# Kernel optimization log

Measured on AMD Instinct MI355X. Metric: run time of the kernel, lower is better.

Reference implementation:

```python
import jax, jax.numpy as jnp
import numpy as np

HEADS = 12
DIM = 768
DH = DIM // HEADS


def setup_inputs() -> dict:
    key = jax.random.key(0)
    k1, k2 = jax.random.split(key)
    z = jax.random.normal(k1, (4, 2048, DIM), dtype=jnp.float32)
    # nn.Linear(dim, 3*dim, bias=False): weight shape [3*dim, dim], y = z @ W.T
    W_qkv = jax.random.normal(k2, (3 * DIM, DIM), dtype=jnp.float32) * (1.0 / np.sqrt(DIM))
    return {"z": z, "W_qkv": W_qkv}


def reference(z, W_qkv):
    b, n, d = z.shape
    qkv = jnp.einsum('bnd,ed->bne', z, W_qkv)  # [b, n, 3*dim]
    # last dim layout is (headNum, m, Dh) per the einops pattern '(headNum m Dh)'
    qkv = qkv.reshape(b, n, HEADS, 3, DH)
    q = jnp.transpose(qkv[:, :, :, 0, :], (0, 2, 1, 3))  # [b, h, n, Dh]
    k = jnp.transpose(qkv[:, :, :, 1, :], (0, 2, 1, 3))
    v = jnp.transpose(qkv[:, :, :, 2, :], (0, 2, 1, 3))
    scores = jnp.einsum('bhqd,bhkd->bhqk', q, k) / np.sqrt(DH).astype(np.float32)
    A = jax.nn.softmax(scores, axis=-1)  # full [b, h, n, n] matrix, as in source
    out = jnp.einsum('bhqk,bhkd->bhqd', A, v)  # [b, h, n, Dh]
    return jnp.transpose(out, (0, 2, 1, 3)).reshape(b, n, d)
```

## Files before the change

kernel.cpp:

```cpp
#include <hip/hip_runtime.h>
#include <hip/hip_bf16.h>
#include <stdint.h>


typedef __attribute__((ext_vector_type(8))) short bf8_t;
typedef __attribute__((ext_vector_type(4))) float f4_t;

__device__ __forceinline__ unsigned short f2bf(float f) {
  union { float f; unsigned u; } x; x.f = f;
  return (unsigned short)((x.u + 0x7fffu + ((x.u >> 16) & 1u)) >> 16);
}
__device__ __forceinline__ unsigned cvt_pk_bf16(float lo, float hi) {
  unsigned r;
  asm("v_cvt_pk_bf16_f32 %0, %1, %2" : "=v"(r) : "v"(lo), "v"(hi));
  return r;
}
__device__ __forceinline__ void gload_lds16(const void* g, void* l) {
  __builtin_amdgcn_global_load_lds(
      (const __attribute__((address_space(1))) void*)g,
      (__attribute__((address_space(3))) void*)l, 16, 0, 0);
}

__global__ __launch_bounds__(256) void cvt_kernel(
    const float* __restrict__ Z, const float* __restrict__ W,
    unsigned short* __restrict__ Zb)
{
  const int idx = blockIdx.x * 256 + threadIdx.x;
  const float* src;
  unsigned short* dst;
  int c;
  if (idx < 786432) { src = Z; dst = Zb; c = idx; }
  else              { src = W; dst = Zb + 6291456; c = idx - 786432; }
  const float4 a0 = *(const float4*)(src + (size_t)c * 8);
  const float4 a1 = *(const float4*)(src + (size_t)c * 8 + 4);
  uint4 pk = { cvt_pk_bf16(a0.x, a0.y), cvt_pk_bf16(a0.z, a0.w),
               cvt_pk_bf16(a1.x, a1.y), cvt_pk_bf16(a1.z, a1.w) };
  *(uint4*)(dst + (size_t)c * 8) = pk;
}

__global__ __launch_bounds__(256, 3) void qkv_gemm_kernel(
    const unsigned short* __restrict__ Zb, const unsigned short* __restrict__ Wb,
    unsigned short* __restrict__ qb, unsigned short* __restrict__ kb,
    unsigned short* __restrict__ vt)
{
  __shared__ __align__(16) unsigned short As[128 * 64];
  __shared__ __align__(16) unsigned short Bs[128 * 64];

  const int tid = threadIdx.x;
  const int w    = tid >> 6;
  const int lane = tid & 63;
  const int g    = lane >> 4;
  const int l15  = lane & 15;
  const int bid0 = blockIdx.y * 18 + blockIdx.x;
  const int bid  = (bid0 & 7) * 144 + (bid0 >> 3);
  const int m0 = (bid / 18) * 128;
  const int n0 = (bid % 18) * 128;
  const int wr = w >> 1, wc = w & 1;

  const int arow = w * 32 + (lane >> 3);
  const int achk = ((lane & 7) ^ (lane >> 3)) * 8;
  const unsigned short* za = Zb + (size_t)(m0 + arow) * 768 + achk;
  const unsigned short* wa = Wb + (size_t)(n0 + arow) * 768 + achk;
  unsigned short* const lza = As + w * 32 * 64;
  unsigned short* const lwa = Bs + w * 32 * 64;

  const f4_t zf = {0.f, 0.f, 0.f, 0.f};
  f4_t acc[4][4];
#pragma unroll
  for (int m = 0; m < 4; ++m)
#pragma unroll
    for (int n = 0; n < 4; ++n) acc[m][n] = zf;

  for (int ks = 0; ks < 12; ++ks) {
    __syncthreads();
#pragma unroll
    for (int r = 0; r < 4; ++r) {
      gload_lds16(za + r * 8 * 768, lza + r * 512);
      gload_lds16(wa + r * 8 * 768, lwa + r * 512);
    }
    za += 64; wa += 64;
    __syncthreads();

#pragma unroll
    for (int s = 0; s < 2; ++s) {
      bf8_t af[4], bfr[4];
#pragma unroll
      for (int m = 0; m < 4; ++m) {
        const int row = wr * 64 + m * 16 + l15;
        af[m] = *(const bf8_t*)(As + row * 64 + (((s * 4 + g) ^ (row & 7)) * 8));
      }
#pragma unroll
      for (int n = 0; n < 4; ++n) {
        const int row = wc * 64 + n * 16 + l15;
        bfr[n] = *(const bf8_t*)(Bs + row * 64 + (((s * 4 + g) ^ (row & 7)) * 8));
      }
      __builtin_amdgcn_s_setprio(1);
#pragma unroll
      for (int m = 0; m < 4; ++m)
#pragma unroll
        for (int n = 0; n < 4; ++n)
          acc[m][n] = __builtin_amdgcn_mfma_f32_16x16x32_bf16(af[m], bfr[n], acc[m][n], 0, 0, 0);
      __builtin_amdgcn_s_setprio(0);
    }
  }

  const float QSCALE = 0.18033688011112042f;
#pragma unroll
  for (int m = 0; m < 4; ++m) {
    const int gi  = m0 + wr * 64 + m * 16 + g * 4;
    const int b   = gi >> 11;
    const int tok = gi & 2047;
#pragma unroll
    for (int n = 0; n < 4; ++n) {
      const int e0  = n0 + wc * 64 + n * 16;
      const int h   = e0 / 192;
      const int rem = e0 - h * 192;
      const int mm  = rem >> 6;
      const int dh  = (rem & 63) + l15;
      if (mm == 2) {
        uint2 pk = { cvt_pk_bf16(acc[m][n][0], acc[m][n][1]),
                     cvt_pk_bf16(acc[m][n][2], acc[m][n][3]) };
        const int pos = ((tok >> 5) & 1) * 32 + ((tok >> 2) & 3) * 8
                      + ((tok >> 4) & 1) * 4;
        const size_t vaddr = ((size_t)(b * 12 + h) * 32 + (tok >> 6)) * 4096
                           + dh * 64 + pos;
        *(uint2*)(vt + vaddr) = pk;
      } else {
        unsigned short* buf = mm ? kb : qb;
        const float sc = mm ? 1.0f : QSCALE;
        const size_t base = ((size_t)((b * 12 + h) * 2048 + tok)) * 64 + dh;
#pragma unroll
        for (int j = 0; j < 4; ++j)
          buf[base + (size_t)j * 64] = f2bf(acc[m][n][j] * sc);
      }
    }
  }
}

__global__ __launch_bounds__(256, 3) void attn_kernel(
    const unsigned short* __restrict__ qb, const unsigned short* __restrict__ kb,
    const unsigned short* __restrict__ vt, float* __restrict__ out)
{
  __shared__ __align__(16) unsigned short Ks[2][64 * 64];
  __shared__ __align__(16) unsigned short Vs[2][64 * 64];

  const int bid = blockIdx.x;
  const int nb  = (bid & 7) * 96 + (bid >> 3);
  const int bh  = nb >> 4;
  const int qt  = nb & 15;
  const int tid = threadIdx.x;
  const int w    = tid >> 6;
  const int lane = tid & 63;
  const int g    = lane >> 4;
  const int l15  = lane & 15;

  const unsigned short* Qh  = qb + (size_t)bh * 2048 * 64;
  const unsigned short* Kh  = kb + (size_t)bh * 2048 * 64;
  const unsigned short* VTh = vt + (size_t)bh * 32 * 4096;

  const int qbase = qt * 128 + w * 32;

  bf8_t qfr[2][2];
#pragma unroll
  for (int qq = 0; qq < 2; ++qq)
#pragma unroll
    for (int s = 0; s < 2; ++s)
      qfr[qq][s] = *(const bf8_t*)(Qh + (size_t)(qbase + qq * 16 + l15) * 64 + s * 32 + g * 8);

  const int xk   = l15 & 7;
  const int offA = l15 * 64 + ((g) ^ xk) * 8;
  const int offB = l15 * 64 + ((4 + g) ^ xk) * 8;

  const size_t dmaoff = (size_t)(w * 16 + (lane >> 3)) * 64
                      + ((lane & 7) ^ (lane >> 3)) * 8;
  const unsigned short* ksrc = Kh + dmaoff;
  const unsigned short* vsrc = VTh + dmaoff;
  const int ldsoff = w * 16 * 64;

  gload_lds16(ksrc,                 &Ks[0][ldsoff]);
  gload_lds16(ksrc + 8 * 64,        &Ks[0][ldsoff + 8 * 64]);
  gload_lds16(vsrc,                 &Vs[0][ldsoff]);
  gload_lds16(vsrc + 8 * 64,        &Vs[0][ldsoff + 8 * 64]);
  gload_lds16(ksrc + 4096,          &Ks[1][ldsoff]);
  gload_lds16(ksrc + 4096 + 8 * 64, &Ks[1][ldsoff + 8 * 64]);
  gload_lds16(vsrc + 4096,          &Vs[1][ldsoff]);
  gload_lds16(vsrc + 4096 + 8 * 64, &Vs[1][ldsoff + 8 * 64]);
  __syncthreads();

  const unsigned short* kdma = ksrc + 2 * 4096;
  const unsigned short* vdma = vsrc + 2 * 4096;

  const f4_t m16 = {-16.f, -16.f, -16.f, -16.f};
  const f4_t zf  = {0.f, 0.f, 0.f, 0.f};
  f4_t accO[2][4];
  unsigned pw[2][8];
  float lsumP[2] = {0.f, 0.f};
#pragma unroll
  for (int qq = 0; qq < 2; ++qq)
#pragma unroll
    for (int nf = 0; nf < 4; ++nf) accO[qq][nf] = zf;

  {
    const unsigned short* pK = &Ks[0][0];
    bf8_t ka0[4][2];
#pragma unroll
    for (int kf = 0; kf < 4; ++kf) {
      ka0[kf][0] = *(const bf8_t*)(pK + offA + kf * 1024);
      ka0[kf][1] = *(const bf8_t*)(pK + offB + kf * 1024);
    }
#pragma unroll
    for (int qq = 0; qq < 2; ++qq) {
      f4_t accS[4];
      __builtin_amdgcn_s_setprio(1);
#pragma unroll
      for (int kf = 0; kf < 4; ++kf) {
        f4_t a = __builtin_amdgcn_mfma_f32_16x16x32_bf16(ka0[kf][0], qfr[qq][0], m16, 0, 0, 0);
        accS[kf] = __builtin_amdgcn_mfma_f32_16x16x32_bf16(ka0[kf][1], qfr[qq][1], a, 0, 0, 0);
      }
      __builtin_amdgcn_s_setprio(0);
      float ps = 0.f;
#pragma unroll
      for (int kf = 0; kf < 4; ++kf) {
        const float p0 = __builtin_amdgcn_exp2f(accS[kf][0]);
        const float p1 = __builtin_amdgcn_exp2f(accS[kf][1]);
        const float p2 = __builtin_amdgcn_exp2f(accS[kf][2]);
        const float p3 = __builtin_amdgcn_exp2f(accS[kf][3]);
        ps += (p0 + p1) + (p2 + p3);
        pw[qq][kf * 2]     = cvt_pk_bf16(p0, p1);
        pw[qq][kf * 2 + 1] = cvt_pk_bf16(p2, p3);
      }
      lsumP[qq] += ps;
    }
  }

  for (int t = 0; t < 32; ++t) {
    const int cur = t & 1;
    const unsigned short* pV = &Vs[cur][0];

    bf8_t vfr[2][4];
#pragma unroll
    for (int nf = 0; nf < 4; ++nf) {
      vfr[0][nf] = *(const bf8_t*)(pV + offA + nf * 1024);
      vfr[1][nf] = *(const bf8_t*)(pV + offB + nf * 1024);
    }

    __syncthreads();

    if (t < 30) {
      gload_lds16(kdma,          &Ks[cur][ldsoff]);
      gload_lds16(kdma + 8 * 64, &Ks[cur][ldsoff + 8 * 64]);
      gload_lds16(vdma,          &Vs[cur][ldsoff]);
      gload_lds16(vdma + 8 * 64, &Vs[cur][ldsoff + 8 * 64]);
      kdma += 4096; vdma += 4096;
    }

    bf8_t ka[4][2];
    if (t < 31) {
      const unsigned short* pK = &Ks[cur ^ 1][0];
#pragma unroll
      for (int kf = 0; kf < 4; ++kf) {
        ka[kf][0] = *(const bf8_t*)(pK + offA + kf * 1024);
        ka[kf][1] = *(const bf8_t*)(pK + offB + kf * 1024);
      }
    }

    __builtin_amdgcn_s_setprio(1);
#pragma unroll
    for (int qq = 0; qq < 2; ++qq) {
      union { bf8_t v[2]; unsigned u[8]; } pa;
#pragma unroll
      for (int i = 0; i < 8; ++i) pa.u[i] = pw[qq][i];
#pragma unroll
      for (int kk = 0; kk < 2; ++kk)
#pragma unroll
        for (int nf = 0; nf < 4; ++nf)
          accO[qq][nf] = __builtin_amdgcn_mfma_f32_16x16x32_bf16(pa.v[kk], vfr[kk][nf], accO[qq][nf], 0, 0, 0);
    }
    __builtin_amdgcn_s_setprio(0);

    if (t < 31) {
#pragma unroll
      for (int qq = 0; qq < 2; ++qq) {
        f4_t accS[4];
        __builtin_amdgcn_s_setprio(1);
#pragma unroll
        for (int kf = 0; kf < 4; ++kf) {
          f4_t a = __builtin_amdgcn_mfma_f32_16x16x32_bf16(ka[kf][0], qfr[qq][0], m16, 0, 0, 0);
          accS[kf] = __builtin_amdgcn_mfma_f32_16x16x32_bf16(ka[kf][1], qfr[qq][1], a, 0, 0, 0);
        }
        __builtin_amdgcn_s_setprio(0);
        float ps = 0.f;
#pragma unroll
        for (int kf = 0; kf < 4; ++kf) {
          const float p0 = __builtin_amdgcn_exp2f(accS[kf][0]);
          const float p1 = __builtin_amdgcn_exp2f(accS[kf][1]);
          const float p2 = __builtin_amdgcn_exp2f(accS[kf][2]);
          const float p3 = __builtin_amdgcn_exp2f(accS[kf][3]);
          ps += (p0 + p1) + (p2 + p3);
          pw[qq][kf * 2]     = cvt_pk_bf16(p0, p1);
          pw[qq][kf * 2 + 1] = cvt_pk_bf16(p2, p3);
        }
        lsumP[qq] += ps;
      }
    }
  }

  const int b = bh / 12, h = bh - (bh / 12) * 12;
#pragma unroll
  for (int qq = 0; qq < 2; ++qq) {
    float ls = lsumP[qq];
    ls += __shfl_xor(ls, 16);
    ls += __shfl_xor(ls, 32);
    const float rl = 1.0f / ls;
    f4_t lv;
#pragma unroll
    for (int j = 0; j < 4; ++j) lv[j] = __shfl(rl, g * 4 + j);
#pragma unroll
    for (int nf = 0; nf < 4; ++nf) {
#pragma unroll
      for (int j = 0; j < 4; ++j) {
        const int qrow = qbase + qq * 16 + g * 4 + j;
        out[((size_t)(b * 2048 + qrow)) * 768 + h * 64 + nf * 16 + l15] = accO[qq][nf][j] * lv[j];
      }
    }
  }
}

extern "C" void kernel_launch(void* const* d_in, const int* in_sizes, int n_in,
                              void* d_out, int out_size, void* d_ws, size_t ws_size,
                              hipStream_t stream) {
  (void)in_sizes; (void)n_in; (void)out_size; (void)ws_size;
  const float* Z = (const float*)d_in[0];
  const float* W = (const float*)d_in[1];
  float* out = (float*)d_out;

  unsigned short* qb = (unsigned short*)d_ws;
  unsigned short* kb = qb + (size_t)48 * 2048 * 64;
  unsigned short* vt = kb + (size_t)48 * 2048 * 64;

  unsigned short* Zb = (unsigned short*)d_out;
  unsigned short* Wb = Zb + (size_t)8192 * 768;

  cvt_kernel<<<dim3(3936), 256, 0, stream>>>(Z, W, Zb);
  qkv_gemm_kernel<<<dim3(18, 64), 256, 0, stream>>>(Zb, Wb, qb, kb, vt);
  attn_kernel<<<dim3(768), 256, 0, stream>>>(qb, kb, vt, out);
}
```

Measured before the change: 104.4 us.

## Double-buffer LDS tiles in QKV GEMM to overlap global loads with MFMA

The QKV projection GEMM now uses two LDS buffers per operand. Two K-stages are preloaded, and each iteration reads all fragments into registers, then issues the async global-to-LDS load for the stage two steps ahead before running the MFMAs. This hides load latency behind compute and drops one barrier per iteration. In exchange, shared memory per block doubles and the launch bound falls from 3 to 2 blocks per CU, which lowers occupancy; fragment offsets are also precomputed.

```diff
diff --git a/kernel.cpp b/kernel.cpp
--- a/kernel.cpp
+++ b/kernel.cpp
@@ -38,13 +38,13 @@
   *(uint4*)(dst + (size_t)c * 8) = pk;
 }
 
-__global__ __launch_bounds__(256, 3) void qkv_gemm_kernel(
+__global__ __launch_bounds__(256, 2) void qkv_gemm_kernel(
     const unsigned short* __restrict__ Zb, const unsigned short* __restrict__ Wb,
     unsigned short* __restrict__ qb, unsigned short* __restrict__ kb,
     unsigned short* __restrict__ vt)
 {
-  __shared__ __align__(16) unsigned short As[128 * 64];
-  __shared__ __align__(16) unsigned short Bs[128 * 64];
+  __shared__ __align__(16) unsigned short As[2][128 * 64];
+  __shared__ __align__(16) unsigned short Bs[2][128 * 64];
 
   const int tid = threadIdx.x;
   const int w    = tid >> 6;
@@ -61,8 +61,13 @@
   const int achk = ((lane & 7) ^ (lane >> 3)) * 8;
   const unsigned short* za = Zb + (size_t)(m0 + arow) * 768 + achk;
   const unsigned short* wa = Wb + (size_t)(n0 + arow) * 768 + achk;
-  unsigned short* const lza = As + w * 32 * 64;
-  unsigned short* const lwa = Bs + w * 32 * 64;
+  const int ldsoff = w * 32 * 64;
+
+  const int xk = l15 & 7;
+  const int offA0 = wr * 4096 + l15 * 64 + ((g) ^ xk) * 8;
+  const int offA1 = wr * 4096 + l15 * 64 + ((4 + g) ^ xk) * 8;
+  const int offB0 = wc * 4096 + l15 * 64 + ((g) ^ xk) * 8;
+  const int offB1 = wc * 4096 + l15 * 64 + ((4 + g) ^ xk) * 8;
 
   const f4_t zf = {0.f, 0.f, 0.f, 0.f};
   f4_t acc[4][4];
@@ -71,37 +76,53 @@
 #pragma unroll
     for (int n = 0; n < 4; ++n) acc[m][n] = zf;
 
+#pragma unroll
+  for (int r = 0; r < 4; ++r) {
+    gload_lds16(za + r * 8 * 768,      &As[0][ldsoff + r * 512]);
+    gload_lds16(wa + r * 8 * 768,      &Bs[0][ldsoff + r * 512]);
+    gload_lds16(za + 64 + r * 8 * 768, &As[1][ldsoff + r * 512]);
+    gload_lds16(wa + 64 + r * 8 * 768, &Bs[1][ldsoff + r * 512]);
+  }
+  za += 128; wa += 128;
+  __syncthreads();
+
   for (int ks = 0; ks < 12; ++ks) {
+    const int cur = ks & 1;
+    const unsigned short* pA = &As[cur][0];
+    const unsigned short* pB = &Bs[cur][0];
+
+    bf8_t af[2][4], bfr[2][4];
+#pragma unroll
+    for (int m = 0; m < 4; ++m) {
+      af[0][m] = *(const bf8_t*)(pA + offA0 + m * 1024);
+      af[1][m] = *(const bf8_t*)(pA + offA1 + m * 1024);
+    }
+#pragma unroll
+    for (int n = 0; n < 4; ++n) {
+      bfr[0][n] = *(const bf8_t*)(pB + offB0 + n * 1024);
+      bfr[1][n] = *(const bf8_t*)(pB + offB1 + n * 1024);
+    }
+
     __syncthreads();
-#pragma unroll
-    for (int r = 0; r < 4; ++r) {
-      gload_lds16(za + r * 8 * 768, lza + r * 512);
-      gload_lds16(wa + r * 8 * 768, lwa + r * 512);
-    }
-    za += 64; wa += 64;
-    __syncthreads();
-
-#pragma unroll
-    for (int s = 0; s < 2; ++s) {
-      bf8_t af[4], bfr[4];
-#pragma unroll
-      for (int m = 0; m < 4; ++m) {
-        const int row = wr * 64 + m * 16 + l15;
-        af[m] = *(const bf8_t*)(As + row * 64 + (((s * 4 + g) ^ (row & 7)) * 8));
-      }
-#pragma unroll
-      for (int n = 0; n < 4; ++n) {
-        const int row = wc * 64 + n * 16 + l15;
-        bfr[n] = *(const bf8_t*)(Bs + row * 64 + (((s * 4 + g) ^ (row & 7)) * 8));
-      }
-      __builtin_amdgcn_s_setprio(1);
+
+    if (ks < 10) {
+#pragma unroll
+      for (int r = 0; r < 4; ++r) {
+        gload_lds16(za + r * 8 * 768, &As[cur][ldsoff + r * 512]);
+        gload_lds16(wa + r * 8 * 768, &Bs[cur][ldsoff + r * 512]);
+      }
+      za += 64; wa += 64;
+    }
+
+    __builtin_amdgcn_s_setprio(1);
+#pragma unroll
+    for (int s = 0; s < 2; ++s)
 #pragma unroll
       for (int m = 0; m < 4; ++m)
 #pragma unroll
         for (int n = 0; n < 4; ++n)
-          acc[m][n] = __builtin_amdgcn_mfma_f32_16x16x32_bf16(af[m], bfr[n], acc[m][n], 0, 0, 0);
-      __builtin_amdgcn_s_setprio(0);
-    }
+          acc[m][n] = __builtin_amdgcn_mfma_f32_16x16x32_bf16(af[s][m], bfr[s][n], acc[m][n], 0, 0, 0);
+    __builtin_amdgcn_s_setprio(0);
   }
 
   const float QSCALE = 0.18033688011112042f;
```

Result: slower. 112.6 us (+7.9%).
